# Kernel tuning notes

Measured on AMD Instinct MI355X. Metric: run time of the kernel, lower is better.

The kernel has to match this reference:

```python
import jax, jax.numpy as jnp
import numpy as np

B, T, C = 2, 2048, 2048
N_HEAD, N_GROUPS, HEAD_SIZE = 16, 4, 128
Q_PER_KV = N_HEAD // N_GROUPS  # 4
N_ELEM = HEAD_SIZE  # rotary_percentage = 1.0
HIDDEN = 4 * C
EPS = 1e-5


def layernorm(x, w, b):
    m = jnp.mean(x, axis=-1, keepdims=True)
    v = jnp.mean(jnp.square(x - m), axis=-1, keepdims=True)
    return (x - m) * jax.lax.rsqrt(v + EPS) * w + b


def apply_rope(x, cos, sin):
    # x: [B, H, T, n_elem]; cos/sin: [T, n_elem] (broadcast over B, H)
    d = x.shape[-1]
    x1, x2 = x[..., : d // 2], x[..., d // 2 :]
    rotated = jnp.concatenate((-x2, x1), axis=-1)
    return x * cos + rotated * sin


def setup_inputs() -> dict:
    key = jax.random.key(0)
    ks = jax.random.split(key, 8)
    x = jax.random.normal(ks[0], (B, T, C), dtype=jnp.float32)
    # rope cache (NeoX/LLaMA half-rotation layout), base 10000
    theta = 1.0 / (10000.0 ** (jnp.arange(0, N_ELEM, 2, dtype=jnp.float32) / N_ELEM))
    idx_theta = jnp.outer(jnp.arange(T, dtype=jnp.float32), theta)  # [T, n_elem//2]
    idx_theta = jnp.concatenate((idx_theta, idx_theta), axis=-1)    # [T, n_elem]
    cos, sin = jnp.cos(idx_theta), jnp.sin(idx_theta)
    mask = jnp.tril(jnp.ones((T, T), dtype=bool))[None, None]  # causal [1,1,T,T]
    s = 0.02
    return {
        "x": x,
        "cos": cos,
        "sin": sin,
        "ln1_w": jnp.ones((C,), jnp.float32),
        "ln1_b": jnp.zeros((C,), jnp.float32),
        "ln2_w": jnp.ones((C,), jnp.float32),
        "ln2_b": jnp.zeros((C,), jnp.float32),
        "w_attn": jax.random.normal(ks[1], (C, (N_HEAD + 2 * N_GROUPS) * HEAD_SIZE), jnp.float32) * s,
        "w_proj": jax.random.normal(ks[2], (C, C), jnp.float32) * s,
        "w_fc": jax.random.normal(ks[3], (C, HIDDEN), jnp.float32) * s,
        "w_mlp_proj": jax.random.normal(ks[4], (HIDDEN, C), jnp.float32) * s,
        "mask": mask,
    }


def reference(x, cos, sin, ln1_w, ln1_b, ln2_w, ln2_b, w_attn, w_proj, w_fc, w_mlp_proj, mask):
    n1 = layernorm(x, ln1_w, ln1_b)
    # fused QKV projection
    qkv = n1 @ w_attn  # [B, T, (H + 2G) * hs]
    qkv = qkv.reshape(B, T, N_GROUPS, Q_PER_KV + 2, HEAD_SIZE)
    q = qkv[:, :, :, :Q_PER_KV]      # [B, T, G, qpk, hs]
    k = qkv[:, :, :, Q_PER_KV]       # [B, T, G, hs]
    v = qkv[:, :, :, Q_PER_KV + 1]   # [B, T, G, hs]
    # q -> [B, H, T, hs] (group-major head order)
    q = q.transpose(0, 2, 3, 1, 4).reshape(B, N_HEAD, T, HEAD_SIZE)
    # k, v -> [B, G, T, hs] then repeat_interleave groups to H heads
    k = jnp.repeat(k.transpose(0, 2, 1, 3), Q_PER_KV, axis=1)  # [B, H, T, hs]
    v = jnp.repeat(v.transpose(0, 2, 1, 3), Q_PER_KV, axis=1)
    # RoPE on the first N_ELEM dims (here full head)
    q = jnp.concatenate((apply_rope(q[..., :N_ELEM], cos, sin), q[..., N_ELEM:]), axis=-1)
    k = jnp.concatenate((apply_rope(k[..., :N_ELEM], cos, sin), k[..., N_ELEM:]), axis=-1)
    scale = 1.0 / np.sqrt(HEAD_SIZE).astype(np.float32)
    att = jnp.einsum("bhtd,bhsd->bhts", q, k) * scale
    att = jnp.where(mask, att, jnp.finfo(att.dtype).min)
    att = jax.nn.softmax(att, axis=-1)
    y = jnp.einsum("bhts,bhsd->bhtd", att, v)
    y = y.transpose(0, 2, 1, 3).reshape(B, T, C)
    h = y @ w_proj
    # non-parallel residual (LLaMA-style): x + attn, then x + mlp(norm2(x))
    x = x + h
    n2 = layernorm(x, ln2_w, ln2_b)
    mlp = jax.nn.gelu(n2 @ w_fc, approximate=False) @ w_mlp_proj
    return x + mlp
```

## Files before the change

### kernel.cpp

```cpp
#include <hip/hip_runtime.h>
#include <stdint.h>
#include <math.h>

#define Tn   2048
#define Cn   2048
#define BTn  4096
#define NQKV 3072
#define HID  8192

typedef unsigned short u16;
typedef float f32x4 __attribute__((ext_vector_type(4)));
typedef short s16x8 __attribute__((ext_vector_type(8)));

__device__ __forceinline__ float b2f(u16 u) { return __uint_as_float(((unsigned)u) << 16); }
__device__ __forceinline__ u16 f2b(float f) {
  unsigned i = __float_as_uint(f);
  return (u16)((i + 0x7fffu + ((i >> 16) & 1u)) >> 16);
}

__device__ __forceinline__ void g2l16(const void* g, void* l) {
  __builtin_amdgcn_global_load_lds((const __attribute__((address_space(1))) unsigned int*)g,
                                   (__attribute__((address_space(3))) unsigned int*)l,
                                   16, 0, 0);
}

__global__ __launch_bounds__(256) void transpose_f2b(const float* __restrict__ in,
                                                     u16* __restrict__ out, int R, int C) {
  __shared__ float tile[32][33];
  int bx = blockIdx.x * 32, by = blockIdx.y * 32;
  int tx = threadIdx.x, ty = threadIdx.y;
  #pragma unroll
  for (int j = 0; j < 32; j += 8)
    tile[ty + j][tx] = in[(size_t)(by + ty + j) * C + bx + tx];
  __syncthreads();
  #pragma unroll
  for (int j = 0; j < 32; j += 8)
    out[(size_t)(bx + ty + j) * R + by + tx] = f2b(tile[tx][ty + j]);
}

__global__ __launch_bounds__(256) void transpose_u16(const u16* __restrict__ in,
                                                     u16* __restrict__ out, int R, int C) {
  __shared__ u16 tile[32][33];
  const size_t zb = (size_t)blockIdx.z * R * C;
  int bx = blockIdx.x * 32, by = blockIdx.y * 32;
  int tx = threadIdx.x, ty = threadIdx.y;
  #pragma unroll
  for (int j = 0; j < 32; j += 8)
    tile[ty + j][tx] = in[zb + (size_t)(by + ty + j) * C + bx + tx];
  __syncthreads();
  #pragma unroll
  for (int j = 0; j < 32; j += 8)
    out[zb + (size_t)(bx + ty + j) * R + by + tx] = tile[tx][ty + j];
}

__global__ __launch_bounds__(256)
void copy_f32(const float* __restrict__ in, float* __restrict__ out) {
  const long i = ((long)blockIdx.x * 256 + threadIdx.x) * 4;
  *(f32x4*)(out + i) = *(const f32x4*)(in + i);
}

__global__ __launch_bounds__(256)
void layernorm_k(const float* __restrict__ x, const float* __restrict__ w,
                 const float* __restrict__ bb, u16* __restrict__ out) {
  __shared__ float red[256];
  __shared__ float sm, sv;
  const int tid = threadIdx.x;
  const long row = blockIdx.x;
  const float* xr = x + row * (long)Cn;
  float v[8];
  float s = 0.f;
  #pragma unroll
  for (int i = 0; i < 8; ++i) { v[i] = xr[i * 256 + tid]; s += v[i]; }
  red[tid] = s; __syncthreads();
  for (int st = 128; st > 0; st >>= 1) { if (tid < st) red[tid] += red[tid + st]; __syncthreads(); }
  if (tid == 0) sm = red[0] * (1.f / Cn);
  __syncthreads();
  const float mean = sm;
  float s2 = 0.f;
  #pragma unroll
  for (int i = 0; i < 8; ++i) { float d = v[i] - mean; s2 += d * d; }
  red[tid] = s2; __syncthreads();
  for (int st = 128; st > 0; st >>= 1) { if (tid < st) red[tid] += red[tid + st]; __syncthreads(); }
  if (tid == 0) sv = rsqrtf(red[0] * (1.f / Cn) + 1e-5f);
  __syncthreads();
  const float rstd = sv;
  #pragma unroll
  for (int i = 0; i < 8; ++i) {
    int c = i * 256 + tid;
    out[row * (long)Cn + c] = f2b((v[i] - mean) * rstd * w[c] + bb[c]);
  }
}

__global__ __launch_bounds__(256)
void rope_split(const u16* __restrict__ qkv, const float* __restrict__ cs,
                const float* __restrict__ sn, u16* __restrict__ q,
                u16* __restrict__ k, u16* __restrict__ v) {
  const long idx = (long)blockIdx.x * 256 + threadIdx.x;
  const int row = (int)(idx / NQKV);
  const int col = (int)(idx % NQKV);
  const int b = row >> 11, t = row & 2047;
  const int g = col / 768, rr = col % 768, s = rr >> 7, d = rr & 127;
  const u16 raw = qkv[idx];
  if (s == 5) { v[((long)(b * 4 + g) * Tn + t) * 128 + d] = raw; return; }
  const float xv = b2f(raw);
  const float x2 = b2f(qkv[idx - d + (d ^ 64)]);
  const float c = cs[t * 128 + d];
  const float si = sn[t * 128 + d];
  const float rot = (d < 64) ? -x2 : x2;
  const float o = xv * c + rot * si;
  if (s == 4) k[((long)(b * 4 + g) * Tn + t) * 128 + d] = f2b(o);
  else        q[((long)(b * 16 + g * 4 + s) * Tn + t) * 128 + d] = f2b(o);
}

__global__ __launch_bounds__(256, 2)
void attn_flash(const u16* __restrict__ q, const u16* __restrict__ k,
                const u16* __restrict__ vt, u16* __restrict__ y) {
  __shared__ __align__(16) u16 Ks[2 * 8192];
  __shared__ __align__(16) u16 Vs[2 * 8192];
  __shared__ __align__(16) u16 Ps[4][2 * 16 * 32];
  const int tid = threadIdx.x, wave = tid >> 6, lane = tid & 63;
  const int fr = lane & 15, quad = lane >> 4;
  const int lr4 = lane >> 2;
  const int su  = ((lr4 >> 3) & 1) << 1;
  const int lcs = (((lane & 3) ^ su) << 3);
  const int ksw = ((fr >> 3) & 1) << 1;
  const int rslot = (quad ^ ksw) << 3;
  const int bx = blockIdx.x, bh = blockIdx.y;
  const int b = bh >> 4, h = bh & 15, g = h >> 2;
  const int bg = b * 4 + g;
  const u16* kg = k + (size_t)bg * Tn * 128;
  const u16* vg = vt + (size_t)bg * 128 * Tn;
  const int q0 = bx * 64 + wave * 16;

  s16x8 qf[4];
  {
    const u16* qrow = q + ((size_t)bh * Tn + q0 + fr) * 128;
    #pragma unroll
    for (int kc = 0; kc < 4; ++kc)
      qf[kc] = *(const s16x8*)(qrow + kc * 32 + quad * 8);
  }
  f32x4 o_acc[8] = {};
  float m_r[4], l_r[4];
  #pragma unroll
  for (int r = 0; r < 4; ++r) { m_r[r] = -1e30f; l_r[r] = 0.f; }
  const float scale = 0.08838834764831845f;

  auto stage_kv = [&](int j0, int bufsel) {
    u16* kd = Ks + bufsel * 8192;
    u16* vd = Vs + bufsel * 8192;
    #pragma unroll
    for (int kc = 0; kc < 4; ++kc)
      g2l16(kg + (size_t)(j0 + wave * 16 + lr4) * 128 + kc * 32 + lcs,
            kd + kc * 2048 + wave * 512);
    #pragma unroll
    for (int kc = 0; kc < 2; ++kc)
      #pragma unroll
      for (int hh = 0; hh < 2; ++hh)
        g2l16(vg + (size_t)(wave * 32 + hh * 16 + lr4) * Tn + j0 + kc * 32 + lcs,
              vd + kc * 4096 + (wave * 32 + hh * 16) * 32);
  };

  stage_kv(0, 0);
  asm volatile("s_waitcnt vmcnt(0)" ::: "memory");
  __builtin_amdgcn_s_barrier();

  int cur = 0;
  for (int step = 0; step <= bx; ++step) {
    const int j0 = step * 64;
    if (step < bx) stage_kv(j0 + 64, cur ^ 1);
    const u16* kcur = Ks + cur * 8192;
    const u16* vcur = Vs + cur * 8192;

    f32x4 s[4] = {};
    __builtin_amdgcn_s_setprio(1);
    #pragma unroll
    for (int kc = 0; kc < 4; ++kc)
      #pragma unroll
      for (int nt = 0; nt < 4; ++nt) {
        s16x8 bf = *(const s16x8*)(kcur + kc * 2048 + (nt * 16 + fr) * 32 + rslot);
        s[nt] = __builtin_amdgcn_mfma_f32_16x16x32_bf16(qf[kc], bf, s[nt], 0, 0, 0);
      }
    __builtin_amdgcn_s_setprio(0);

    const bool diag = (step == bx);
    #pragma unroll
    for (int r = 0; r < 4; ++r) {
      float vmax = -1e30f;
      #pragma unroll
      for (int nt = 0; nt < 4; ++nt) {
        float sv = s[nt][r] * scale;
        if (diag && (j0 + nt * 16 + fr) > (q0 + quad * 4 + r)) sv = -1e30f;
        s[nt][r] = sv;
        vmax = fmaxf(vmax, sv);
      }
      #pragma unroll
      for (int mk = 1; mk < 16; mk <<= 1) vmax = fmaxf(vmax, __shfl_xor(vmax, mk, 64));
      const float mnew = fmaxf(m_r[r], vmax);
      const float alpha = __expf(m_r[r] - mnew);
      float rsum = 0.f;
      #pragma unroll
      for (int nt = 0; nt < 4; ++nt) {
        float pv = __expf(s[nt][r] - mnew);
        s[nt][r] = pv; rsum += pv;
      }
      #pragma unroll
      for (int mk = 1; mk < 16; mk <<= 1) rsum += __shfl_xor(rsum, mk, 64);
      l_r[r] = l_r[r] * alpha + rsum;
      m_r[r] = mnew;
      #pragma unroll
      for (int nt = 0; nt < 8; ++nt) o_acc[nt][r] *= alpha;
    }

    u16* pw = Ps[wave];
    #pragma unroll
    for (int nt = 0; nt < 4; ++nt) {
      const int col = nt * 16 + fr, pan = col >> 5, cc = col & 31;
      #pragma unroll
      for (int r = 0; r < 4; ++r) {
        const int prow = quad * 4 + r;
        pw[pan * 512 + prow * 32 + (cc ^ (((prow >> 3) & 1) << 4))] = f2b(s[nt][r]);
      }
    }
    #pragma unroll
    for (int kc = 0; kc < 2; ++kc) {
      s16x8 af = *(const s16x8*)(pw + kc * 512 + fr * 32 + rslot);
      __builtin_amdgcn_s_setprio(1);
      #pragma unroll
      for (int nt = 0; nt < 8; ++nt) {
        s16x8 bf = *(const s16x8*)(vcur + kc * 4096 + (nt * 16 + fr) * 32 + rslot);
        o_acc[nt] = __builtin_amdgcn_mfma_f32_16x16x32_bf16(af, bf, o_acc[nt], 0, 0, 0);
      }
      __builtin_amdgcn_s_setprio(0);
    }

    asm volatile("s_waitcnt vmcnt(0) lgkmcnt(0)" ::: "memory");
    __builtin_amdgcn_s_barrier();
    cur ^= 1;
  }

  #pragma unroll
  for (int r = 0; r < 4; ++r) {
    const float inv = 1.f / l_r[r];
    const size_t row = (size_t)(b * Tn + q0 + quad * 4 + r) * Cn + h * 128;
    #pragma unroll
    for (int nt = 0; nt < 8; ++nt)
      y[row + nt * 16 + fr] = f2b(o_acc[nt][r] * inv);
  }
}

#define BAR  __builtin_amdgcn_s_barrier()

template <int EPI>
__global__ __launch_bounds__(512, 2)
void gemm256(const u16* __restrict__ A, const u16* __restrict__ Bt,
             const float* __restrict__ res, u16* __restrict__ ob,
             float* __restrict__ of, int N, int Kl, int ld, int num_n) {
  __shared__ __align__(16) u16 S[65536];
  char* Sb = (char*)S;

  const long koff = (long)blockIdx.y * Kl;
  A += koff; Bt += koff;

  const int pid = blockIdx.x;
  const int xcd = pid & 7, idx = pid >> 3;
  const int jj = idx & 3;
  const int gp = (idx >> 2) * 8 + xcd;
  const int npc = num_n >> 1;
  const int pr = gp / npc, pc = gp - pr * npc;
  const long m0 = (long)(pr * 2 + (jj >> 1)) * 256;
  const long n0 = (long)(pc * 2 + (jj & 1)) * 256;

  const int tid = (int)threadIdx.x;
  const int wave = tid >> 6, lane = tid & 63;
  const int wr = wave >> 2, wc = wave & 3;
  const int fr = lane & 15, quad = lane >> 4;
  const int fragoff = (fr * 64 + quad * 16) ^ (((fr >> 3) & 1) << 5);
  const int aBase = wr * 16384;
  const int bBase = 65536 + (wc >> 1) * 16384 + ((wc & 1) << 13);

  int srow[2], skcb[2];
  #pragma unroll
  for (int rr = 0; rr < 2; ++rr) {
    const int d = rr * 8192 + wave * 1024 + lane * 16;
    const int l = d ^ (((d >> 9) & 1) << 5);
    srow[rr] = ((l >> 11) << 4) | ((l >> 6) & 15);
    skcb[rr] = (((l >> 10) & 1) << 6) | (l & 63);
  }
  auto stage = [&](const u16* __restrict__ src, long grow0, int kt, int regionByte) {
    #pragma unroll
    for (int rr = 0; rr < 2; ++rr)
      g2l16((const char*)src + (grow0 + srow[rr]) * (long)ld * 2 + (long)kt * 128 + skcb[rr],
            Sb + regionByte + rr * 8192 + wave * 1024);
  };

  const int nk = Kl >> 6;

  stage(A,  m0,       0, 0);
  stage(A,  m0 + 128, 0, 16384);
  stage(Bt, n0,       0, 65536);
  stage(Bt, n0 + 128, 0, 81920);
  asm volatile("s_waitcnt vmcnt(0)" ::: "memory");
  BAR;

  f32x4 acc[8][4] = {};

  for (int t = 0; t < nk; ++t) {
    const int bufB = (t & 1) * 32768;
    const int obufB = 32768 - bufB;
    const bool vn = (t + 1 < nk);

    s16x8 br[4][2];
    #pragma unroll
    for (int n_ = 0; n_ < 4; ++n_)
      #pragma unroll
      for (int k_ = 0; k_ < 2; ++k_)
        br[n_][k_] = *(const s16x8*)(Sb + bufB + bBase + (n_ << 11) + (k_ << 10) + fragoff);

    if (vn) {
      stage(A,  m0,       t + 1, obufB);
      stage(A,  m0 + 128, t + 1, obufB + 16384);
      stage(Bt, n0,       t + 1, 65536 + obufB);
      stage(Bt, n0 + 128, t + 1, 65536 + obufB + 16384);
    }

    #pragma unroll
    for (int m_ = 0; m_ < 8; ++m_) {
      const char* arow = Sb + bufB + aBase + (m_ << 11) + fragoff;
      s16x8 a0 = *(const s16x8*)(arow);
      s16x8 a1 = *(const s16x8*)(arow + 1024);
      __builtin_amdgcn_s_setprio(1);
      #pragma unroll
      for (int n_ = 0; n_ < 4; ++n_) {
        acc[m_][n_] = __builtin_amdgcn_mfma_f32_16x16x32_bf16(a0, br[n_][0], acc[m_][n_], 0, 0, 0);
        acc[m_][n_] = __builtin_amdgcn_mfma_f32_16x16x32_bf16(a1, br[n_][1], acc[m_][n_], 0, 0, 0);
      }
      __builtin_amdgcn_s_setprio(0);
    }

    asm volatile("s_waitcnt vmcnt(0) lgkmcnt(0)" ::: "memory");
    BAR;
  }

  #pragma unroll
  for (int mi = 0; mi < 8; ++mi)
    #pragma unroll
    for (int ni = 0; ni < 4; ++ni)
      #pragma unroll
      for (int r = 0; r < 4; ++r) {
        const long row = m0 + wr * 128 + mi * 16 + quad * 4 + r;
        const long col = n0 + wc * 64 + ni * 16 + fr;
        const long idx2 = row * N + col;
        const float vv = acc[mi][ni][r];
        if (EPI == 0) ob[idx2] = f2b(vv);
        else if (EPI == 1) of[idx2] = vv + res[idx2];
        else if (EPI == 2) ob[idx2] = f2b(0.5f * vv * (1.0f + erff(vv * 0.70710678118654752f)));
        else atomicAdd(&of[idx2], vv);
      }
}

extern "C" void kernel_launch(void* const* d_in, const int* in_sizes, int n_in,
                              void* d_out, int out_size, void* d_ws, size_t ws_size,
                              hipStream_t stream) {
  (void)in_sizes; (void)n_in; (void)out_size; (void)ws_size;
  const float* x      = (const float*)d_in[0];
  const float* cosb   = (const float*)d_in[1];
  const float* sinb   = (const float*)d_in[2];
  const float* ln1w   = (const float*)d_in[3];
  const float* ln1b   = (const float*)d_in[4];
  const float* ln2w   = (const float*)d_in[5];
  const float* ln2b   = (const float*)d_in[6];
  const float* w_attn = (const float*)d_in[7];
  const float* w_proj = (const float*)d_in[8];
  const float* w_fc   = (const float*)d_in[9];
  const float* w_mp   = (const float*)d_in[10];
  float* out = (float*)d_out;

  char* p = (char*)d_ws;
  auto alloc = [&](size_t bytes) { char* r = p; p += (bytes + 255) & ~(size_t)255; return (void*)r; };
  u16*  wT_attn = (u16*)alloc((size_t)NQKV * Cn * 2);
  u16*  wT_proj = (u16*)alloc((size_t)Cn * Cn * 2);
  u16*  wT_fc   = (u16*)alloc((size_t)HID * Cn * 2);
  u16*  wT_mp   = (u16*)alloc((size_t)Cn * HID * 2);
  u16*  n12     = (u16*)alloc((size_t)BTn * Cn * 2);
  u16*  qkv     = (u16*)alloc((size_t)BTn * NQKV * 2);
  u16*  qb      = (u16*)alloc((size_t)2 * 16 * Tn * 128 * 2);
  u16*  kb      = (u16*)alloc((size_t)2 * 4 * Tn * 128 * 2);
  u16*  vb      = (u16*)alloc((size_t)2 * 4 * Tn * 128 * 2);
  float* x1     = (float*)alloc((size_t)BTn * Cn * 4);
  u16*  hbuf    = (u16*)alloc((size_t)BTn * HID * 2);
  u16*  vt      = n12;

  dim3 tb(32, 8);
  transpose_f2b<<<dim3(NQKV / 32, Cn / 32), tb, 0, stream>>>(w_attn, wT_attn, Cn, NQKV);
  transpose_f2b<<<dim3(Cn / 32, Cn / 32), tb, 0, stream>>>(w_proj, wT_proj, Cn, Cn);
  transpose_f2b<<<dim3(HID / 32, Cn / 32), tb, 0, stream>>>(w_fc, wT_fc, Cn, HID);
  transpose_f2b<<<dim3(Cn / 32, HID / 32), tb, 0, stream>>>(w_mp, wT_mp, HID, Cn);

  layernorm_k<<<BTn, 256, 0, stream>>>(x, ln1w, ln1b, n12);
  gemm256<0><<<(BTn / 256) * (NQKV / 256), 512, 0, stream>>>(n12, wT_attn, nullptr, qkv, nullptr, NQKV, Cn, Cn, NQKV / 256);
  rope_split<<<(int)(((long)BTn * NQKV) / 256), 256, 0, stream>>>(qkv, cosb, sinb, qb, kb, vb);
  transpose_u16<<<dim3(128 / 32, Tn / 32, 8), tb, 0, stream>>>(vb, vt, Tn, 128);
  attn_flash<<<dim3(Tn / 64, 32), 256, 0, stream>>>(qb, kb, vt, qkv );
  copy_f32<<<(int)(((long)BTn * Cn) / 1024), 256, 0, stream>>>(x, x1);
  gemm256<3><<<dim3((BTn / 256) * (Cn / 256), 2), 512, 0, stream>>>(qkv, wT_proj, nullptr, nullptr, x1, Cn, Cn / 2, Cn, Cn / 256);
  layernorm_k<<<BTn, 256, 0, stream>>>(x1, ln2w, ln2b, n12);
  gemm256<2><<<(BTn / 256) * (HID / 256), 512, 0, stream>>>(n12, wT_fc, nullptr, hbuf, nullptr, HID, Cn, Cn, HID / 256);
  copy_f32<<<(int)(((long)BTn * Cn) / 1024), 256, 0, stream>>>(x1, out);
  gemm256<3><<<dim3((BTn / 256) * (Cn / 256), 2), 512, 0, stream>>>(hbuf, wT_mp, nullptr, nullptr, out, Cn, HID / 2, HID, Cn / 256);
}
```

Baseline: 900.2 us.

## Shrink GEMM tiles to 128x256 with K-step 32 for higher occupancy

Replaces the 256x256, K=64 GEMM tile with a 128x256 tile and a 32-wide K step. LDS use drops from 128KB to 48KB and launch bounds rise to 4 blocks per CU. Each wave now holds a 4x4 accumulator grid instead of 8x4, and the grids launch twice as many blocks. The aim is more latency hiding and better wave fill on the GEMMs. The cost is lower arithmetic intensity per tile, twice as many barriers per unit of K, and possibly a worse swizzle mapping for the smaller tile.

```diff
diff --git a/kernel.cpp b/kernel.cpp
--- a/kernel.cpp
+++ b/kernel.cpp
@@ -251,11 +251,11 @@
 #define BAR  __builtin_amdgcn_s_barrier()
 
 template <int EPI>
-__global__ __launch_bounds__(512, 2)
-void gemm256(const u16* __restrict__ A, const u16* __restrict__ Bt,
+__global__ __launch_bounds__(512, 4)
+void gemm128(const u16* __restrict__ A, const u16* __restrict__ Bt,
              const float* __restrict__ res, u16* __restrict__ ob,
              float* __restrict__ of, int N, int Kl, int ld, int num_n) {
-  __shared__ __align__(16) u16 S[65536];
+  __shared__ __align__(16) u16 S[24576];
   char* Sb = (char*)S;
 
   const long koff = (long)blockIdx.y * Kl;
@@ -267,7 +267,7 @@
   const int gp = (idx >> 2) * 8 + xcd;
   const int npc = num_n >> 1;
   const int pr = gp / npc, pc = gp - pr * npc;
-  const long m0 = (long)(pr * 2 + (jj >> 1)) * 256;
+  const long m0 = (long)(pr * 2 + (jj >> 1)) * 128;
   const long n0 = (long)(pc * 2 + (jj & 1)) * 256;
 
   const int tid = (int)threadIdx.x;
@@ -275,79 +275,71 @@
   const int wr = wave >> 2, wc = wave & 3;
   const int fr = lane & 15, quad = lane >> 4;
   const int fragoff = (fr * 64 + quad * 16) ^ (((fr >> 3) & 1) << 5);
-  const int aBase = wr * 16384;
-  const int bBase = 65536 + (wc >> 1) * 16384 + ((wc & 1) << 13);
-
-  int srow[2], skcb[2];
-  #pragma unroll
-  for (int rr = 0; rr < 2; ++rr) {
-    const int d = rr * 8192 + wave * 1024 + lane * 16;
+  const long ld2 = (long)ld * 2;
+
+  const int dA = tid * 16;
+  const int lA = dA ^ (((dA >> 9) & 1) << 5);
+  const int srowA = lA >> 6, skA = lA & 63;
+  int srowB[2], skB[2];
+  #pragma unroll
+  for (int s = 0; s < 2; ++s) {
+    const int d = s * 8192 + tid * 16;
     const int l = d ^ (((d >> 9) & 1) << 5);
-    srow[rr] = ((l >> 11) << 4) | ((l >> 6) & 15);
-    skcb[rr] = (((l >> 10) & 1) << 6) | (l & 63);
-  }
-  auto stage = [&](const u16* __restrict__ src, long grow0, int kt, int regionByte) {
-    #pragma unroll
-    for (int rr = 0; rr < 2; ++rr)
-      g2l16((const char*)src + (grow0 + srow[rr]) * (long)ld * 2 + (long)kt * 128 + skcb[rr],
-            Sb + regionByte + rr * 8192 + wave * 1024);
+    srowB[s] = l >> 6; skB[s] = l & 63;
+  }
+  auto stageA = [&](int kt, int buf) {
+    g2l16((const char*)A + (m0 + srowA) * ld2 + (long)kt * 64 + skA,
+          Sb + buf * 8192 + wave * 1024);
   };
-
-  const int nk = Kl >> 6;
-
-  stage(A,  m0,       0, 0);
-  stage(A,  m0 + 128, 0, 16384);
-  stage(Bt, n0,       0, 65536);
-  stage(Bt, n0 + 128, 0, 81920);
+  auto stageB = [&](int kt, int buf) {
+    #pragma unroll
+    for (int s = 0; s < 2; ++s)
+      g2l16((const char*)Bt + (n0 + srowB[s]) * ld2 + (long)kt * 64 + skB[s],
+            Sb + 16384 + buf * 16384 + s * 8192 + wave * 1024);
+  };
+
+  const int nk = Kl >> 5;
+
+  stageA(0, 0);
+  stageB(0, 0);
   asm volatile("s_waitcnt vmcnt(0)" ::: "memory");
   BAR;
 
-  f32x4 acc[8][4] = {};
+  f32x4 acc[4][4] = {};
 
   for (int t = 0; t < nk; ++t) {
-    const int bufB = (t & 1) * 32768;
-    const int obufB = 32768 - bufB;
+    const int buf = t & 1;
     const bool vn = (t + 1 < nk);
 
-    s16x8 br[4][2];
-    #pragma unroll
-    for (int n_ = 0; n_ < 4; ++n_)
-      #pragma unroll
-      for (int k_ = 0; k_ < 2; ++k_)
-        br[n_][k_] = *(const s16x8*)(Sb + bufB + bBase + (n_ << 11) + (k_ << 10) + fragoff);
-
-    if (vn) {
-      stage(A,  m0,       t + 1, obufB);
-      stage(A,  m0 + 128, t + 1, obufB + 16384);
-      stage(Bt, n0,       t + 1, 65536 + obufB);
-      stage(Bt, n0 + 128, t + 1, 65536 + obufB + 16384);
-    }
-
-    #pragma unroll
-    for (int m_ = 0; m_ < 8; ++m_) {
-      const char* arow = Sb + bufB + aBase + (m_ << 11) + fragoff;
-      s16x8 a0 = *(const s16x8*)(arow);
-      s16x8 a1 = *(const s16x8*)(arow + 1024);
-      __builtin_amdgcn_s_setprio(1);
-      #pragma unroll
-      for (int n_ = 0; n_ < 4; ++n_) {
-        acc[m_][n_] = __builtin_amdgcn_mfma_f32_16x16x32_bf16(a0, br[n_][0], acc[m_][n_], 0, 0, 0);
-        acc[m_][n_] = __builtin_amdgcn_mfma_f32_16x16x32_bf16(a1, br[n_][1], acc[m_][n_], 0, 0, 0);
-      }
-      __builtin_amdgcn_s_setprio(0);
-    }
+    s16x8 afr[4], bfr[4];
+    #pragma unroll
+    for (int mi = 0; mi < 4; ++mi)
+      afr[mi] = *(const s16x8*)(Sb + buf * 8192 + (wr * 4 + mi) * 1024 + fragoff);
+    #pragma unroll
+    for (int ni = 0; ni < 4; ++ni)
+      bfr[ni] = *(const s16x8*)(Sb + 16384 + buf * 16384 + (wc * 4 + ni) * 1024 + fragoff);
+
+    if (vn) { stageA(t + 1, buf ^ 1); stageB(t + 1, buf ^ 1); }
+
+    __builtin_amdgcn_s_setprio(1);
+    #pragma unroll
+    for (int mi = 0; mi < 4; ++mi)
+      #pragma unroll
+      for (int ni = 0; ni < 4; ++ni)
+        acc[mi][ni] = __builtin_amdgcn_mfma_f32_16x16x32_bf16(afr[mi], bfr[ni], acc[mi][ni], 0, 0, 0);
+    __builtin_amdgcn_s_setprio(0);
 
     asm volatile("s_waitcnt vmcnt(0) lgkmcnt(0)" ::: "memory");
     BAR;
   }
 
   #pragma unroll
-  for (int mi = 0; mi < 8; ++mi)
+  for (int mi = 0; mi < 4; ++mi)
     #pragma unroll
     for (int ni = 0; ni < 4; ++ni)
       #pragma unroll
       for (int r = 0; r < 4; ++r) {
-        const long row = m0 + wr * 128 + mi * 16 + quad * 4 + r;
+        const long row = m0 + wr * 64 + mi * 16 + quad * 4 + r;
         const long col = n0 + wc * 64 + ni * 16 + fr;
         const long idx2 = row * N + col;
         const float vv = acc[mi][ni][r];
@@ -397,14 +389,14 @@
   transpose_f2b<<<dim3(Cn / 32, HID / 32), tb, 0, stream>>>(w_mp, wT_mp, HID, Cn);
 
   layernorm_k<<<BTn, 256, 0, stream>>>(x, ln1w, ln1b, n12);
-  gemm256<0><<<(BTn / 256) * (NQKV / 256), 512, 0, stream>>>(n12, wT_attn, nullptr, qkv, nullptr, NQKV, Cn, Cn, NQKV / 256);
+  gemm128<0><<<(BTn / 128) * (NQKV / 256), 512, 0, stream>>>(n12, wT_attn, nullptr, qkv, nullptr, NQKV, Cn, Cn, NQKV / 256);
   rope_split<<<(int)(((long)BTn * NQKV) / 256), 256, 0, stream>>>(qkv, cosb, sinb, qb, kb, vb);
   transpose_u16<<<dim3(128 / 32, Tn / 32, 8), tb, 0, stream>>>(vb, vt, Tn, 128);
   attn_flash<<<dim3(Tn / 64, 32), 256, 0, stream>>>(qb, kb, vt, qkv );
   copy_f32<<<(int)(((long)BTn * Cn) / 1024), 256, 0, stream>>>(x, x1);
-  gemm256<3><<<dim3((BTn / 256) * (Cn / 256), 2), 512, 0, stream>>>(qkv, wT_proj, nullptr, nullptr, x1, Cn, Cn / 2, Cn, Cn / 256);
+  gemm128<3><<<dim3((BTn / 128) * (Cn / 256), 2), 512, 0, stream>>>(qkv, wT_proj, nullptr, nullptr, x1, Cn, Cn / 2, Cn, Cn / 256);
   layernorm_k<<<BTn, 256, 0, stream>>>(x1, ln2w, ln2b, n12);
-  gemm256<2><<<(BTn / 256) * (HID / 256), 512, 0, stream>>>(n12, wT_fc, nullptr, hbuf, nullptr, HID, Cn, Cn, HID / 256);
+  gemm128<2><<<(BTn / 128) * (HID / 256), 512, 0, stream>>>(n12, wT_fc, nullptr, hbuf, nullptr, HID, Cn, Cn, HID / 256);
   copy_f32<<<(int)(((long)BTn * Cn) / 1024), 256, 0, stream>>>(x1, out);
-  gemm256<3><<<dim3((BTn / 256) * (Cn / 256), 2), 512, 0, stream>>>(hbuf, wT_mp, nullptr, nullptr, out, Cn, HID / 2, HID, Cn / 256);
-}
+  gemm128<3><<<dim3((BTn / 128) * (Cn / 256), 2), 512, 0, stream>>>(hbuf, wT_mp, nullptr, nullptr, out, Cn, HID / 2, HID, Cn / 256);
+}
```

Measured after the change: 934.6 us. +3.8%, slower.
